# Performance work log

Hardware: AMD Instinct MI355X
Metric: run time of the kernel (lower is better)

## Reference

```python
import jax, jax.numpy as jnp
import numpy as np

L, S, B, E, H, FF = 512, 2048, 4, 1024, 16, 2048
HD = E // H  # 64


def _layernorm(x, g, b, eps=1e-5):
    m = jnp.mean(x, axis=-1, keepdims=True)
    v = jnp.mean((x - m) ** 2, axis=-1, keepdims=True)
    return (x - m) * jax.lax.rsqrt(v + eps) * g + b


def _decoder(tgt, memory, pos, query_pos,
             in_proj_w, in_proj_b, out_w, out_b,
             cq_w, cq_b, ck_w, ck_b, cv_w, cv_b,
             down_w, down_b, lin1_w, lin1_b, lin2_w, lin2_b,
             n1_g, n1_b, n2_g, n2_b, n3_g, n3_b):
    Lq, Bb, Em = tgt.shape
    scale = 1.0 / np.sqrt(HD).astype(np.float32)
    # --- self attention (torch nn.MultiheadAttention, eval mode, no masks) ---
    qk_in = tgt + query_pos
    Wq, Wk, Wv = jnp.split(in_proj_w, 3, axis=0)
    bq, bk, bv = jnp.split(in_proj_b, 3)
    q = (qk_in @ Wq.T + bq).reshape(Lq, Bb, H, HD)
    k = (qk_in @ Wk.T + bk).reshape(Lq, Bb, H, HD)
    v = (tgt @ Wv.T + bv).reshape(Lq, Bb, H, HD)
    attn = jax.nn.softmax(jnp.einsum('lbhd,mbhd->bhlm', q, k) * scale, axis=-1)
    ctx = jnp.einsum('bhlm,mbhd->lbhd', attn, v).reshape(Lq, Bb, Em)
    tgt = _layernorm(tgt + ctx @ out_w.T + out_b, n1_g, n1_b)
    # --- custom cross attention; inputs permuted to [B, E, N] (Conv1d k=1 == matmul) ---
    qc = jnp.einsum('oe,lbe->bol', cq_w, tgt + query_pos) + cq_b[None, :, None]
    kc = jnp.einsum('oe,sbe->bos', ck_w, memory + pos) + ck_b[None, :, None]
    vc = jnp.einsum('oe,sbe->bos', cv_w, memory) + cv_b[None, :, None]
    # view(B, head_dim, num_heads, N): channel axis splits as (HD, H)
    qc = qc.reshape(Bb, HD, H, -1)
    kc = kc.reshape(Bb, HD, H, -1)
    vc = vc.reshape(Bb, HD, H, -1)
    # scores_2[b,d,h,m] = kc[b,d,h,m] * sum_{d',n} qc[b,d',h,n] kc[b,d',h,m] / sqrt(HD)
    # (einsum('abcd,aced->abcd', key, scores_1) broadcasts key over the summed n axis)
    s1sum = jnp.einsum('bdh,bdhm->bhm', qc.sum(-1), kc) * scale
    prob = jax.nn.softmax(kc * s1sum[:, None, :, :], axis=-1)        # [B,HD,H,S]
    o = jnp.einsum('bnhm,bdhm->bdhn', prob, vc)                       # [B,HD,H,HD]
    o = (o @ down_w.T + down_b).reshape(Bb, Em, 1)                    # Linear HD->1, then view
    tgt = _layernorm(tgt + jnp.transpose(o, (2, 0, 1)), n2_g, n2_b)   # [1,B,E] broadcasts over L
    # --- FFN ---
    ff = jax.nn.relu(tgt @ lin1_w.T + lin1_b) @ lin2_w.T + lin2_b
    return _layernorm(tgt + ff, n3_g, n3_b)


def setup_inputs() -> dict:
    key = jax.random.key(0)
    ks = jax.random.split(key, 16)
    def nrm(k, shape, s=0.02):
        return (s * jax.random.normal(k, shape)).astype(jnp.float32)
    z = lambda *s: jnp.zeros(s, jnp.float32)
    return dict(
        tgt=nrm(ks[0], (L, B, E), 1.0),
        memory=nrm(ks[1], (S, B, E), 1.0),
        pos=nrm(ks[2], (S, B, E), 1.0),
        query_pos=nrm(ks[3], (L, B, E), 1.0),
        in_proj_w=nrm(ks[4], (3 * E, E)), in_proj_b=z(3 * E),
        out_w=nrm(ks[5], (E, E)), out_b=z(E),
        cq_w=nrm(ks[6], (E, E)), cq_b=z(E),
        ck_w=nrm(ks[7], (E, E)), ck_b=z(E),
        cv_w=nrm(ks[8], (E, E)), cv_b=z(E),
        down_w=nrm(ks[9], (1, HD)), down_b=z(1),
        lin1_w=nrm(ks[10], (FF, E)), lin1_b=z(FF),
        lin2_w=nrm(ks[11], (E, FF)), lin2_b=z(E),
        n1_g=jnp.ones((E,), jnp.float32), n1_b=z(E),
        n2_g=jnp.ones((E,), jnp.float32), n2_b=z(E),
        n3_g=jnp.ones((E,), jnp.float32), n3_b=z(E),
    )


def reference(tgt, memory, pos, query_pos,
              in_proj_w, in_proj_b, out_w, out_b,
              cq_w, cq_b, ck_w, ck_b, cv_w, cv_b,
              down_w, down_b, lin1_w, lin1_b, lin2_w, lin2_b,
              n1_g, n1_b, n2_g, n2_b, n3_g, n3_b):
    return _decoder(tgt, memory, pos, query_pos,
                    in_proj_w, in_proj_b, out_w, out_b,
                    cq_w, cq_b, ck_w, ck_b, cv_w, cv_b,
                    down_w, down_b, lin1_w, lin1_b, lin2_w, lin2_b,
                    n1_g, n1_b, n2_g, n2_b, n3_g, n3_b)
```

## Files before the change

### kernel.cpp

```cpp
#include <hip/hip_runtime.h>
#include <hip/hip_bf16.h>

typedef __hip_bfloat16 bf16;
typedef short short8 __attribute__((ext_vector_type(8)));
typedef float f32x4 __attribute__((ext_vector_type(4)));

#define Lq 512
#define Sm 2048
#define Bb 4
#define Ee 1024
#define Hh 16
#define FFd 2048
#define HDd 64

static __device__ __forceinline__ float b2f(bf16 x) { return __bfloat162float(x); }
static __device__ __forceinline__ bf16 f2b(float x) { return __float2bfloat16(x); }
static __device__ __forceinline__ unsigned short bits(bf16 x) {
    return __builtin_bit_cast(unsigned short, x);
}
static __device__ __forceinline__ float us2f(unsigned short u) {
    return b2f(__builtin_bit_cast(bf16, u));
}

static __device__ __forceinline__ void gload16(const void* g, void* l) {
    __builtin_amdgcn_global_load_lds(
        (const __attribute__((address_space(1))) unsigned int*)g,
        (__attribute__((address_space(3))) unsigned int*)l, 16, 0, 0);
}

__global__ __launch_bounds__(512, 2)
void kcvc_gemm(const bf16* __restrict__ wk, const bf16* __restrict__ wv,
               const bf16* __restrict__ mp, const bf16* __restrict__ mo,
               bf16* __restrict__ kc, bf16* __restrict__ vc,
               const float* __restrict__ kb, const float* __restrict__ vb)
{
    constexpr int BK = 64;
    __shared__ bf16 lA[2][256 * BK];
    __shared__ bf16 lB[2][256 * BK];

    const int tid  = threadIdx.x;
    const int lane = tid & 63;
    const int wm = (tid >> 6) >> 2;
    const int wn = (tid >> 6) & 3;

    int bid = (blockIdx.x & 7) * 32 + (blockIdx.x >> 3);
    const int bx = bid & 3;
    const int by = (bid >> 2) & 7;
    const int z  = bid >> 5;

    const bool isv = z >= 4;
    const int  b   = isv ? z - 4 : z;
    const bf16*  A    = isv ? wv : wk;
    const bf16*  B    = (isv ? mo : mp) + b * 1024;
    bf16*        C    = (isv ? vc : kc) + (long)b * 2097152;
    const float* bias = isv ? vb : kb;

    const int m0 = bx * 256, n0 = by * 256;
    const bf16* Abase = A + (long)m0 * 1024;
    const bf16* Bbase = B + (long)n0 * 4096;

    const int kgrp = lane >> 4, l16 = lane & 15;
    const int rsw = l16 & 7;

    auto stage = [&](int buf, int k0) {
#pragma unroll
        for (int r = 0; r < 4; r++) {
            int c = r * 512 + tid;
            int row = c >> 3;
            int ss = (c & 7) ^ (row & 7);
            gload16(Abase + (long)row * 1024 + k0 + ss * 8, &lA[buf][c * 8]);
        }
#pragma unroll
        for (int r = 0; r < 4; r++) {
            int c = r * 512 + tid;
            int row = c >> 3;
            int ss = (c & 7) ^ (row & 7);
            gload16(Bbase + (long)row * 4096 + k0 + ss * 8, &lB[buf][c * 8]);
        }
    };

    f32x4 acc[8][4];
#pragma unroll
    for (int i = 0; i < 8; i++)
#pragma unroll
        for (int j = 0; j < 4; j++) acc[i][j] = f32x4{0.f, 0.f, 0.f, 0.f};

    stage(0, 0);
    asm volatile("s_waitcnt vmcnt(0)" ::: "memory");
    __builtin_amdgcn_s_barrier();

    constexpr int NT = 16;
    for (int t = 0; t < NT; t++) {
        if (t + 1 < NT) stage((t + 1) & 1, (t + 1) * BK);

        const bf16* la = lA[t & 1];
        const bf16* lb = lB[t & 1];
#pragma unroll
        for (int h = 0; h < 2; h++) {
            const int sd = ((h * 4 + kgrp) ^ rsw) * 8;
            short8 af[8], bv[4];
#pragma unroll
            for (int i = 0; i < 8; i++)
                af[i] = *(const short8*)&la[(wm * 128 + i * 16 + l16) * BK + sd];
#pragma unroll
            for (int j = 0; j < 4; j++)
                bv[j] = *(const short8*)&lb[(wn * 64 + j * 16 + l16) * BK + sd];
            __builtin_amdgcn_s_setprio(1);
#pragma unroll
            for (int i = 0; i < 8; i++)
#pragma unroll
                for (int j = 0; j < 4; j++)
                    acc[i][j] = __builtin_amdgcn_mfma_f32_16x16x32_bf16(af[i], bv[j], acc[i][j], 0, 0, 0);
            __builtin_amdgcn_s_setprio(0);
        }

        asm volatile("s_waitcnt vmcnt(0)" ::: "memory");
        __builtin_amdgcn_s_barrier();
    }

#pragma unroll
    for (int i = 0; i < 8; i++) {
#pragma unroll
        for (int j = 0; j < 4; j++) {
#pragma unroll
            for (int r = 0; r < 4; r++) {
                int row = m0 + wm * 128 + i * 16 + kgrp * 4 + r;
                int col = n0 + wn * 64 + j * 16 + l16;
                float v = acc[i][j][r] + bias[row];
                float v2 = __shfl_xor(v, 1);
                if (!(l16 & 1)) {
                    unsigned int pk = (unsigned int)bits(f2b(v)) |
                                      ((unsigned int)bits(f2b(v2)) << 16);
                    *(unsigned int*)&C[(long)row * 2048 + col] = pk;
                }
            }
        }
    }
}

__global__ __launch_bounds__(512, 2)
void flash_attn(const bf16* __restrict__ qk, const bf16* __restrict__ vt,
                bf16* __restrict__ ctx)
{
    __shared__ bf16 lQ[128 * 64];
    __shared__ bf16 lK[2][64 * 64];
    __shared__ bf16 lV[2][64 * 64];
    __shared__ bf16 lP[128 * 64];
    __shared__ float scb[128];

    const int tid  = threadIdx.x;
    const int lane = tid & 63;
    const int wq   = tid >> 6;
    const int kgrp = lane >> 4, l16 = lane & 15;

    const int qt = blockIdx.x & 3;
    const int bh = blockIdx.x >> 2;
    const int b = bh >> 4, h = bh & 15;
    const int L0 = qt * 128;

#pragma unroll
    for (int it = 0; it < 2; it++) {
        int c = it * 512 + tid;
        int rr = c >> 3, sl = c & 7, ss = sl ^ (rr & 7);
        gload16(qk + ((long)(L0 + rr) * 4 + b) * 2048 + h * 64 + ss * 8,
                &lQ[(it * 512 + wq * 64) * 8]);
    }

    auto stageKV = [&](int buf, int st) {
        int rr = tid >> 3, sl = tid & 7, ss = sl ^ (rr & 7);
        gload16(qk + ((long)(st * 64 + rr) * 4 + b) * 2048 + 1024 + h * 64 + ss * 8,
                &lK[buf][(wq * 64) * 8]);
        gload16(vt + ((long)(b * 1024 + h * 64 + rr)) * 512 + st * 64 + ss * 8,
                &lV[buf][(wq * 64) * 8]);
    };

    auto frag = [&](const bf16* base, int row, int kk) {
        return *(const short8*)&base[row * 64 + (((kk * 4 + kgrp) ^ (l16 & 7)) * 8)];
    };

    f32x4 acc_o[4];
#pragma unroll
    for (int j = 0; j < 4; j++) acc_o[j] = f32x4{0.f, 0.f, 0.f, 0.f};
    float m_run = -1e30f, l_run = 0.f;

    stageKV(0, 0);
    asm volatile("s_waitcnt vmcnt(0)" ::: "memory");
    __builtin_amdgcn_s_barrier();

    int buf = 0;
    for (int st = 0; st < 8; st++) {
        if (st < 7) stageKV(buf ^ 1, st + 1);

        f32x4 accs[4];
#pragma unroll
        for (int fm = 0; fm < 4; fm++) accs[fm] = f32x4{0.f, 0.f, 0.f, 0.f};
        __builtin_amdgcn_s_setprio(1);
#pragma unroll
        for (int kk = 0; kk < 2; kk++) {
            short8 bq = frag(lQ, wq * 16 + l16, kk);
#pragma unroll
            for (int fm = 0; fm < 4; fm++) {
                short8 af = frag(lK[buf], fm * 16 + l16, kk);
                accs[fm] = __builtin_amdgcn_mfma_f32_16x16x32_bf16(af, bq, accs[fm], 0, 0, 0);
            }
        }
        __builtin_amdgcn_s_setprio(0);

        float v[4][4], p[4][4];
        float tmax = -1e30f;
#pragma unroll
        for (int fm = 0; fm < 4; fm++)
#pragma unroll
            for (int r = 0; r < 4; r++) {
                v[fm][r] = accs[fm][r] * 0.125f;
                tmax = fmaxf(tmax, v[fm][r]);
            }
        tmax = fmaxf(tmax, __shfl_xor(tmax, 16));
        tmax = fmaxf(tmax, __shfl_xor(tmax, 32));
        float m_new = fmaxf(m_run, tmax);
        float sc = __expf(m_run - m_new);
        float sum = 0.f;
#pragma unroll
        for (int fm = 0; fm < 4; fm++)
#pragma unroll
            for (int r = 0; r < 4; r++) {
                p[fm][r] = __expf(v[fm][r] - m_new);
                sum += p[fm][r];
            }
        sum += __shfl_xor(sum, 16);
        sum += __shfl_xor(sum, 32);
        l_run = l_run * sc + sum;
        m_run = m_new;

        if (!kgrp) scb[wq * 16 + l16] = sc;
        asm volatile("s_waitcnt lgkmcnt(0)" ::: "memory");
        __builtin_amdgcn_sched_barrier(0);
        float sc2[4];
#pragma unroll
        for (int r = 0; r < 4; r++) sc2[r] = scb[wq * 16 + kgrp * 4 + r];
#pragma unroll
        for (int fn = 0; fn < 4; fn++)
#pragma unroll
            for (int r = 0; r < 4; r++) acc_o[fn][r] *= sc2[r];

#pragma unroll
        for (int fm = 0; fm < 4; fm++) {
            int l = wq * 16 + l16;
            int sp = (fm * 2 + (kgrp >> 1)) ^ (l16 & 7);
            uint2 pk;
            pk.x = (unsigned int)bits(f2b(p[fm][0])) | ((unsigned int)bits(f2b(p[fm][1])) << 16);
            pk.y = (unsigned int)bits(f2b(p[fm][2])) | ((unsigned int)bits(f2b(p[fm][3])) << 16);
            *(uint2*)&lP[l * 64 + sp * 8 + (kgrp & 1) * 4] = pk;
        }
        asm volatile("s_waitcnt lgkmcnt(0)" ::: "memory");
        __builtin_amdgcn_sched_barrier(0);

        __builtin_amdgcn_s_setprio(1);
#pragma unroll
        for (int kk = 0; kk < 2; kk++) {
            short8 ap = frag(lP, wq * 16 + l16, kk);
#pragma unroll
            for (int fn = 0; fn < 4; fn++) {
                short8 bvf = frag(lV[buf], fn * 16 + l16, kk);
                acc_o[fn] = __builtin_amdgcn_mfma_f32_16x16x32_bf16(ap, bvf, acc_o[fn], 0, 0, 0);
            }
        }
        __builtin_amdgcn_s_setprio(0);

        asm volatile("s_waitcnt vmcnt(0)" ::: "memory");
        __builtin_amdgcn_s_barrier();
        buf ^= 1;
    }

    if (!kgrp) scb[wq * 16 + l16] = 1.f / l_run;
    asm volatile("s_waitcnt lgkmcnt(0)" ::: "memory");
    __builtin_amdgcn_sched_barrier(0);
    float inv[4];
#pragma unroll
    for (int r = 0; r < 4; r++) inv[r] = scb[wq * 16 + kgrp * 4 + r];
#pragma unroll
    for (int fn = 0; fn < 4; fn++) {
#pragma unroll
        for (int r = 0; r < 4; r++) {
            int lg = L0 + wq * 16 + kgrp * 4 + r;
            int d  = fn * 16 + l16;
            float vv = acc_o[fn][r] * inv[r];
            float v2 = __shfl_xor(vv, 1);
            if (!(l16 & 1)) {
                unsigned int pk = (unsigned int)bits(f2b(vv)) |
                                  ((unsigned int)bits(f2b(v2)) << 16);
                *(unsigned int*)&ctx[((long)lg * 4 + b) * 1024 + h * 64 + d] = pk;
            }
        }
    }
}

template<int BM, int BN>
__global__ __launch_bounds__(256)
void gemm_nt(const bf16* __restrict__ A, const bf16* __restrict__ Bw,
             float* __restrict__ Cf, bf16* __restrict__ Cb,
             const float* __restrict__ bias,
             const bf16* __restrict__ A2, const bf16* __restrict__ B2,
             bf16* __restrict__ Cb2, const float* __restrict__ bias2,
             int gx, int gy,
             int K, long lda, long ldb, long ldc,
             long sA1, long sA2, long sB1, long sB2, long sC1, long sC2,
             int zdiv, int zsplit, int nsplit, float alpha, int mode, int mode2)
{
    constexpr int BK = 32;
    constexpr int RA = BM / 64, RB = BN / 64;
    constexpr int NLOADS = RA + RB;
    __shared__ bf16 lA[3][BM * BK];
    __shared__ bf16 lB[3][BN * BK];

    const int tid  = threadIdx.x;
    const int lane = tid & 63;
    const int wave = tid >> 6;
    const int wm = wave >> 1, wn = wave & 1;
    constexpr int RM = BM / 2, RN = BN / 2;
    constexpr int FM = RM / 16, FN = RN / 16;

    const int nwg = gridDim.x;
    const int cpx = nwg >> 3;
    int bid = (blockIdx.x & 7) * cpx + (blockIdx.x >> 3);
    const int bx = bid % gx;
    int tmp = bid / gx;
    const int by = tmp % gy;
    const int z  = tmp / gy;

    const int m0 = bx * BM;
    const int n0 = by * BN;

    const bool use2 = (z >= zsplit) || (n0 >= nsplit);
    const int  zz   = (z >= zsplit) ? z - zsplit : z;
    const bf16*  Ap = (use2 && A2)    ? A2    : A;
    const bf16*  Bp = (use2 && B2)    ? B2    : Bw;
    const float* bp = (use2 && bias2) ? bias2 : bias;
    const int    md = use2 ? mode2 : mode;
    bf16*        Co = (use2 && Cb2)   ? Cb2   : Cb;

    const long offA = (long)(zz / zdiv) * sA1 + (long)(zz % zdiv) * sA2;
    const long offB = (long)(zz / zdiv) * sB1 + (long)(zz % zdiv) * sB2;
    const long offC = (long)(zz / zdiv) * sC1 + (long)(zz % zdiv) * sC2;

    const bf16* Abase = Ap + offA + (long)m0 * lda;
    const bf16* Bbase = Bp + offB + (long)n0 * ldb;

    const int kgrp = lane >> 4;
    const int l16  = lane & 15;

    const int swz   = (l16 >> 1) & 3;
    const int slotA = (kgrp ^ swz) * 8;

    auto stage = [&](int buf, int k0) {
#pragma unroll
        for (int r = 0; r < RA; r++) {
            int c = r * 256 + wave * 64 + lane;
            int row = c >> 2;
            int sslot = (c & 3) ^ ((row >> 1) & 3);
            gload16(Abase + (long)row * lda + k0 + sslot * 8,
                    &lA[buf][(r * 256 + wave * 64) * 8]);
        }
#pragma unroll
        for (int r = 0; r < RB; r++) {
            int c = r * 256 + wave * 64 + lane;
            int row = c >> 2;
            int sslot = (c & 3) ^ ((row >> 1) & 3);
            gload16(Bbase + (long)row * ldb + k0 + sslot * 8,
                    &lB[buf][(r * 256 + wave * 64) * 8]);
        }
    };

    f32x4 acc[FM][FN];
#pragma unroll
    for (int i = 0; i < FM; i++)
#pragma unroll
        for (int j = 0; j < FN; j++) acc[i][j] = f32x4{0.f, 0.f, 0.f, 0.f};

    const int nt = K / BK;
    stage(0, 0);
    if (nt > 1) {
        stage(1, BK);
        asm volatile("s_waitcnt vmcnt(%0)" :: "n"(NLOADS) : "memory");
    } else {
        asm volatile("s_waitcnt vmcnt(0)" ::: "memory");
    }
    __builtin_amdgcn_s_barrier();

    for (int t = 0; t < nt; t++) {
        const int cur = t % 3;
        if (t + 2 < nt) stage((t + 2) % 3, (t + 2) * BK);

        short8 af[FM], bv[FN];
#pragma unroll
        for (int i = 0; i < FM; i++)
            af[i] = *(const short8*)&lA[cur][(wm * RM + i * 16 + l16) * BK + slotA];
#pragma unroll
        for (int j = 0; j < FN; j++)
            bv[j] = *(const short8*)&lB[cur][(wn * RN + j * 16 + l16) * BK + slotA];
        __builtin_amdgcn_s_setprio(1);
#pragma unroll
        for (int i = 0; i < FM; i++)
#pragma unroll
            for (int j = 0; j < FN; j++)
                acc[i][j] = __builtin_amdgcn_mfma_f32_16x16x32_bf16(af[i], bv[j], acc[i][j], 0, 0, 0);
        __builtin_amdgcn_s_setprio(0);

        if (t + 2 < nt) {
            asm volatile("s_waitcnt vmcnt(%0)" :: "n"(NLOADS) : "memory");
        } else {
            asm volatile("s_waitcnt vmcnt(0)" ::: "memory");
        }
        __builtin_amdgcn_s_barrier();
    }

#pragma unroll
    for (int i = 0; i < FM; i++) {
#pragma unroll
        for (int j = 0; j < FN; j++) {
#pragma unroll
            for (int r = 0; r < 4; r++) {
                int row = m0 + wm * RM + i * 16 + kgrp * 4 + r;
                int col = n0 + wn * RN + j * 16 + l16;
                float v = alpha * acc[i][j][r] + (bp ? bp[col] : 0.f);
                float v2 = __shfl_xor(v, 1);
                if (md == 0) {
                    if (!(l16 & 1)) {
                        float2 pv = {v, v2};
                        *(float2*)&Cf[offC + (long)row * ldc + col] = pv;
                    }
                } else if (md == 1) {
                    if (!(l16 & 1)) {
                        unsigned int pk = (unsigned int)bits(f2b(v)) |
                                          ((unsigned int)bits(f2b(v2)) << 16);
                        *(unsigned int*)&Co[offC + (long)row * ldc + col] = pk;
                    }
                } else if (md == 2) {
                    if (!(l16 & 1)) {
                        unsigned int pk = (unsigned int)bits(f2b(fmaxf(v, 0.f))) |
                                          ((unsigned int)bits(f2b(fmaxf(v2, 0.f))) << 16);
                        *(unsigned int*)&Co[offC + (long)row * ldc + col] = pk;
                    }
                } else {
                    int o = col - nsplit;
                    Cb2[((long)(row & 3) * 1024 + o) * 512 + (row >> 2)] = f2b(v);
                }
            }
        }
    }
}

struct Cvt2Seg { const float* a; const float* b; bf16* d; bf16* d2; int nblk; };
struct Cvt2Args { Cvt2Seg s[8]; };

__global__ __launch_bounds__(256)
void cvt_kernel(Cvt2Args args)
{
    for (int ci = blockIdx.x; ci < 10240; ci += 2048) {
        int rem = ci;
        int si = 0;
        while (si < 7 && rem >= args.s[si].nblk) { rem -= args.s[si].nblk; si++; }
        Cvt2Seg sg = args.s[si];
        const long i = (long)rem * 2048 + threadIdx.x * 8;

        float4 a0 = *(const float4*)(sg.a + i);
        float4 a1 = *(const float4*)(sg.a + i + 4);
        float4 s0 = a0, s1 = a1;
        if (sg.b) {
            float4 b0 = *(const float4*)(sg.b + i);
            float4 b1 = *(const float4*)(sg.b + i + 4);
            s0.x += b0.x; s0.y += b0.y; s0.z += b0.z; s0.w += b0.w;
            s1.x += b1.x; s1.y += b1.y; s1.z += b1.z; s1.w += b1.w;
        }
        short8 u;
        u[0] = (short)bits(f2b(s0.x)); u[1] = (short)bits(f2b(s0.y));
        u[2] = (short)bits(f2b(s0.z)); u[3] = (short)bits(f2b(s0.w));
        u[4] = (short)bits(f2b(s1.x)); u[5] = (short)bits(f2b(s1.y));
        u[6] = (short)bits(f2b(s1.z)); u[7] = (short)bits(f2b(s1.w));
        *(short8*)((unsigned short*)sg.d + i) = u;
        if (sg.d2) {
            short8 w;
            w[0] = (short)bits(f2b(a0.x)); w[1] = (short)bits(f2b(a0.y));
            w[2] = (short)bits(f2b(a0.z)); w[3] = (short)bits(f2b(a0.w));
            w[4] = (short)bits(f2b(a1.x)); w[5] = (short)bits(f2b(a1.y));
            w[6] = (short)bits(f2b(a1.z)); w[7] = (short)bits(f2b(a1.w));
            *(short8*)((unsigned short*)sg.d2 + i) = w;
        }
    }
}

__global__ __launch_bounds__(256)
void ln_kernel(const float* __restrict__ x, const bf16* __restrict__ xB,
               const float* __restrict__ res, const float* __restrict__ resb,
               const float* __restrict__ g, const float* __restrict__ be,
               float* __restrict__ outF, bf16* __restrict__ outB)
{
    long row = blockIdx.x;
    int tid = threadIdx.x, lane = tid & 63, w = tid >> 6;
    float vv[4];
    if (x) {
        float4 xv = *(const float4*)(x + row * 1024 + tid * 4);
        vv[0] = xv.x; vv[1] = xv.y; vv[2] = xv.z; vv[3] = xv.w;
    } else {
        ushort4 xv = *(const ushort4*)((const unsigned short*)xB + row * 1024 + tid * 4);
        vv[0] = us2f(xv.x); vv[1] = us2f(xv.y); vv[2] = us2f(xv.z); vv[3] = us2f(xv.w);
    }
    if (res) {
        float4 rv = *(const float4*)(res + row * 1024 + tid * 4);
        vv[0] += rv.x; vv[1] += rv.y; vv[2] += rv.z; vv[3] += rv.w;
    }
    if (resb) {
        float4 rv = *(const float4*)(resb + (row & 3) * 1024 + tid * 4);
        vv[0] += rv.x; vv[1] += rv.y; vv[2] += rv.z; vv[3] += rv.w;
    }
    float s = vv[0] + vv[1] + vv[2] + vv[3];
    float q = vv[0] * vv[0] + vv[1] * vv[1] + vv[2] * vv[2] + vv[3] * vv[3];
    __shared__ float rs[4], rq[4];
    for (int o = 32; o; o >>= 1) { s += __shfl_xor(s, o); q += __shfl_xor(q, o); }
    if (!lane) { rs[w] = s; rq[w] = q; }
    __syncthreads();
    s = rs[0] + rs[1] + rs[2] + rs[3];
    q = rq[0] + rq[1] + rq[2] + rq[3];
    float mean = s * (1.f / 1024.f);
    float var  = q * (1.f / 1024.f) - mean * mean;
    float rstd = rsqrtf(var + 1e-5f);
    float4 gv = *(const float4*)(g + tid * 4);
    float4 bv = *(const float4*)(be + tid * 4);
    float o0 = (vv[0] - mean) * rstd * gv.x + bv.x;
    float o1 = (vv[1] - mean) * rstd * gv.y + bv.y;
    float o2 = (vv[2] - mean) * rstd * gv.z + bv.z;
    float o3 = (vv[3] - mean) * rstd * gv.w + bv.w;
    if (outF) {
        float4 ov = {o0, o1, o2, o3};
        *(float4*)(outF + row * 1024 + tid * 4) = ov;
    }
    if (outB) {
        ushort4 u;
        u.x = bits(f2b(o0)); u.y = bits(f2b(o1));
        u.z = bits(f2b(o2)); u.w = bits(f2b(o3));
        *reinterpret_cast<ushort4*>((unsigned short*)outB + row * 1024 + tid * 4) = u;
    }
}

__global__ __launch_bounds__(256)
void asum_part_kernel(const float* __restrict__ t1, const float* __restrict__ qp,
                      float* __restrict__ part)
{
    int blk = blockIdx.x;
    int lc = blk >> 4, b = (blk >> 2) & 3, ec = blk & 3;
    int e = ec * 256 + threadIdx.x;
    float acc = 0.f;
#pragma unroll 4
    for (int l = lc * 32; l < lc * 32 + 32; l++) {
        long idx = ((long)(l * 4 + b)) * 1024 + e;
        acc += t1[idx] + qp[idx];
    }
    part[(lc * 4 + b) * 1024 + e] = acc;
}

__global__ __launch_bounds__(256)
void asum_reduce_kernel(const float* __restrict__ part, float* __restrict__ asum)
{
    int b = blockIdx.x >> 2, ec = blockIdx.x & 3;
    int e = ec * 256 + threadIdx.x;
    float acc = 0.f;
#pragma unroll
    for (int lc = 0; lc < 16; lc++) acc += part[(lc * 4 + b) * 1024 + e];
    asum[b * 1024 + e] = acc;
}

__global__ __launch_bounds__(256)
void qsum_kernel(const float* __restrict__ cqw, const float* __restrict__ cqb,
                 const float* __restrict__ asum, float* __restrict__ qsum)
{
    int o = blockIdx.x * 4 + (threadIdx.x >> 6);
    int lane = threadIdx.x & 63;
    float a0 = 0, a1 = 0, a2 = 0, a3 = 0;
    for (int j = 0; j < 16; j++) {
        int e = lane + j * 64;
        float wv = cqw[(long)o * 1024 + e];
        a0 += wv * asum[e];
        a1 += wv * asum[1024 + e];
        a2 += wv * asum[2048 + e];
        a3 += wv * asum[3072 + e];
    }
    for (int t = 32; t; t >>= 1) {
        a0 += __shfl_xor(a0, t); a1 += __shfl_xor(a1, t);
        a2 += __shfl_xor(a2, t); a3 += __shfl_xor(a3, t);
    }
    if (!lane) {
        float bb = 512.f * cqb[o];
        qsum[o] = a0 + bb; qsum[1024 + o] = a1 + bb;
        qsum[2048 + o] = a2 + bb; qsum[3072 + o] = a3 + bb;
    }
}

__global__ __launch_bounds__(256)
void s1_kernel(const bf16* __restrict__ kc, const float* __restrict__ qsum,
               float* __restrict__ s1)
{
    int bh = blockIdx.x, b = bh >> 4, h = bh & 15;
    int m = blockIdx.y * 256 + threadIdx.x;
    __shared__ float qd[64];
    if (threadIdx.x < 64) qd[threadIdx.x] = qsum[b * 1024 + threadIdx.x * 16 + h];
    __syncthreads();
    const bf16* kcb = kc + (long)b * 2048 * 1024 + (long)h * 2048 + m;
    float acc = 0.f;
#pragma unroll 8
    for (int d = 0; d < 64; d++) acc += qd[d] * b2f(kcb[(long)d * 16 * 2048]);
    s1[(long)bh * 2048 + m] = acc * 0.125f;
}

__global__ __launch_bounds__(256)
void bsum_kernel(const bf16* __restrict__ kc, const float* __restrict__ s1,
                 float* __restrict__ rmax, float* __restrict__ rsum)
{
    int bh = blockIdx.x >> 6, n = blockIdx.x & 63;
    int b = bh >> 4, h = bh & 15;
    int tid = threadIdx.x, lane = tid & 63, w = tid >> 6;
    const bf16* row = kc + (long)b * 2048 * 1024 + (long)(n * 16 + h) * 2048;
    const float* s1r = s1 + (long)bh * 2048;
    float t[8];
    float mx = -1e30f;
#pragma unroll
    for (int i = 0; i < 8; i++) {
        int m = tid + i * 256;
        t[i] = b2f(row[m]) * s1r[m];
        mx = fmaxf(mx, t[i]);
    }
    __shared__ float redm[4], reds[4];
    for (int o = 32; o; o >>= 1) mx = fmaxf(mx, __shfl_xor(mx, o));
    if (!lane) redm[w] = mx;
    __syncthreads();
    mx = fmaxf(fmaxf(redm[0], redm[1]), fmaxf(redm[2], redm[3]));
    float s = 0.f;
#pragma unroll
    for (int i = 0; i < 8; i++) s += __expf(t[i] - mx);
    for (int o = 32; o; o >>= 1) s += __shfl_xor(s, o);
    if (!lane) reds[w] = s;
    __syncthreads();
    if (!tid) {
        rmax[bh * 64 + n] = mx;
        rsum[bh * 64 + n] = reds[0] + reds[1] + reds[2] + reds[3];
    }
}

__global__ __launch_bounds__(256)
void wpr_kernel(const bf16* __restrict__ kc, const float* __restrict__ s1,
                const float* __restrict__ rmax, const float* __restrict__ rsum,
                const float* __restrict__ dw, float* __restrict__ wpr)
{
    int bh = blockIdx.x, b = bh >> 4, h = bh & 15;
    int m = blockIdx.y * 256 + threadIdx.x;
    __shared__ float cf[64], cm[64];
    if (threadIdx.x < 64) {
        cf[threadIdx.x] = dw[threadIdx.x] / rsum[bh * 64 + threadIdx.x];
        cm[threadIdx.x] = rmax[bh * 64 + threadIdx.x];
    }
    __syncthreads();
    float s1v = s1[(long)bh * 2048 + m];
    const bf16* kcb = kc + (long)b * 2048 * 1024 + (long)h * 2048 + m;
    float acc = 0.f;
#pragma unroll 8
    for (int n = 0; n < 64; n++)
        acc += cf[n] * __expf(b2f(kcb[(long)n * 16 * 2048]) * s1v - cm[n]);
    wpr[(long)bh * 2048 + m] = acc;
}

__global__ __launch_bounds__(256)
void cout_kernel(const bf16* __restrict__ vc, const float* __restrict__ wpr,
                 const float* __restrict__ db, float* __restrict__ outs)
{
    int bh = blockIdx.x >> 2, dg = blockIdx.x & 3;
    int b = bh >> 4, h = bh & 15;
    int tid = threadIdx.x, lane = tid & 63, w = tid >> 6;
    __shared__ float lwpr[2048];
#pragma unroll
    for (int i = 0; i < 8; i++) lwpr[tid + i * 256] = wpr[(long)bh * 2048 + tid + i * 256];
    __syncthreads();
#pragma unroll
    for (int dd = 0; dd < 4; dd++) {
        int d = dg * 16 + w * 4 + dd;
        int o = d * 16 + h;
        const bf16* vrow = vc + (long)b * 2048 * 1024 + (long)o * 2048;
        float acc = 0.f;
#pragma unroll
        for (int j = 0; j < 4; j++) {
            int m = j * 512 + lane * 8;
            short8 vv = *(const short8*)&vrow[m];
#pragma unroll
            for (int k = 0; k < 8; k++) {
                bf16 bb = __builtin_bit_cast(bf16, (unsigned short)vv[k]);
                acc += lwpr[m + k] * b2f(bb);
            }
        }
        for (int t2 = 32; t2; t2 >>= 1) acc += __shfl_xor(acc, t2);
        if (!lane) outs[b * 1024 + o] = acc + db[0];
    }
}

extern "C" void kernel_launch(void* const* d_in, const int* in_sizes, int n_in,
                              void* d_out, int out_size, void* d_ws, size_t ws_size,
                              hipStream_t stream)
{
    const float* tgt  = (const float*)d_in[0];
    const float* mem  = (const float*)d_in[1];
    const float* pos  = (const float*)d_in[2];
    const float* qp   = (const float*)d_in[3];
    const float* ipw  = (const float*)d_in[4];
    const float* ipb  = (const float*)d_in[5];
    const float* outw = (const float*)d_in[6];
    const float* outb = (const float*)d_in[7];
    const float* cqw  = (const float*)d_in[8];
    const float* cqb  = (const float*)d_in[9];
    const float* ckw  = (const float*)d_in[10];
    const float* ckb  = (const float*)d_in[11];
    const float* cvw  = (const float*)d_in[12];
    const float* cvb  = (const float*)d_in[13];
    const float* dww  = (const float*)d_in[14];
    const float* dwb  = (const float*)d_in[15];
    const float* l1w  = (const float*)d_in[16];
    const float* l1b  = (const float*)d_in[17];
    const float* l2w  = (const float*)d_in[18];
    const float* l2b  = (const float*)d_in[19];
    const float* n1g  = (const float*)d_in[20];
    const float* n1b  = (const float*)d_in[21];
    const float* n2g  = (const float*)d_in[22];
    const float* n2b  = (const float*)d_in[23];
    const float* n3g  = (const float*)d_in[24];
    const float* n3b  = (const float*)d_in[25];

    char* ws = (char*)d_ws;
    auto MB = [](long x) { return x << 20; };
    bf16* w_ip    = (bf16*)(ws + MB(0));
    bf16* w_out   = (bf16*)(ws + MB(6));
    bf16* w_ck    = (bf16*)(ws + MB(8));
    bf16* w_cv    = (bf16*)(ws + MB(10));
    bf16* w_l1    = (bf16*)(ws + MB(12));
    bf16* w_l2    = (bf16*)(ws + MB(16));
    bf16* qkin    = (bf16*)(ws + MB(20));
    bf16* tgtb    = (bf16*)(ws + MB(24));
    bf16* memposb = (bf16*)(ws + MB(28));
    bf16* memb    = (bf16*)(ws + MB(44));
    bf16* qkbuf   = (bf16*)(ws + MB(60));
    bf16* vtb     = (bf16*)(ws + MB(68));
    bf16* kcb     = (bf16*)(ws + MB(72));
    bf16* ctxb    = (bf16*)(ws + MB(104));
    bf16* atmpb   = (bf16*)(ws + MB(108));
    float* s1buf  = (float*)(ws + MB(108));
    float* wprbuf = (float*)(ws + MB(109));
    float* rmax   = (float*)(ws + MB(110));
    float* rsum   = (float*)(ws + MB(110) + (64 << 10));
    float* part   = (float*)(ws + MB(111));
    float* tgt1   = (float*)(ws + MB(116));
    float* asum   = (float*)(ws + MB(124));
    float* qsum   = (float*)(ws + MB(125));
    bf16* vcb     = (bf16*)(ws + MB(126));
    float* outs   = (float*)(ws + MB(142));
    float* tgt2   = (float*)(ws + MB(143));
    bf16* tgt2b   = (bf16*)(ws + MB(151));
    bf16* ff1b    = (bf16*)(ws + MB(155));
    bf16* ff2b    = (bf16*)(ws + MB(163));

    const int BIGZ = 1000000, BIGN = 1 << 30;

    Cvt2Args ca{};
    ca.s[0] = {ipw,  nullptr, w_ip,    nullptr, 1536};
    ca.s[1] = {outw, nullptr, w_out,   nullptr, 512};
    ca.s[2] = {ckw,  nullptr, w_ck,    nullptr, 512};
    ca.s[3] = {cvw,  nullptr, w_cv,    nullptr, 512};
    ca.s[4] = {l1w,  nullptr, w_l1,    nullptr, 1024};
    ca.s[5] = {l2w,  nullptr, w_l2,    nullptr, 1024};
    ca.s[6] = {tgt,  qp,      qkin,    tgtb,    1024};
    ca.s[7] = {mem,  pos,     memposb, memb,    4096};
    cvt_kernel<<<dim3(2048, 1, 1), 256, 0, stream>>>(ca);

    gemm_nt<64, 128><<<dim3(768, 1, 1), 256, 0, stream>>>(
        qkin, w_ip, nullptr, qkbuf, ipb,
        tgtb, nullptr, vtb, nullptr,
        32, 24,
        1024, 1024, 1024, 2048,
        0, 0, 0, 0, 0, 0, 1, BIGZ, 2048, 1.f, 1, 3);

    flash_attn<<<dim3(256, 1, 1), 512, 0, stream>>>(qkbuf, vtb, ctxb);

    gemm_nt<64, 128><<<dim3(256, 1, 1), 256, 0, stream>>>(
        ctxb, w_out, nullptr, atmpb, outb,
        nullptr, nullptr, nullptr, nullptr,
        32, 8,
        1024, 1024, 1024, 1024,
        0, 0, 0, 0, 0, 0, 1, BIGZ, BIGN, 1.f, 1, 1);

    ln_kernel<<<dim3(2048, 1, 1), 256, 0, stream>>>(
        nullptr, atmpb, tgt, nullptr, n1g, n1b, tgt1, nullptr);

    asum_part_kernel<<<dim3(256, 1, 1), 256, 0, stream>>>(tgt1, qp, part);
    asum_reduce_kernel<<<dim3(16, 1, 1), 256, 0, stream>>>(part, asum);
    qsum_kernel<<<dim3(256, 1, 1), 256, 0, stream>>>(cqw, cqb, asum, qsum);

    kcvc_gemm<<<dim3(256, 1, 1), 512, 0, stream>>>(
        w_ck, w_cv, memposb, memb, kcb, vcb, ckb, cvb);

    s1_kernel<<<dim3(64, 8, 1), 256, 0, stream>>>(kcb, qsum, s1buf);
    bsum_kernel<<<dim3(4096, 1, 1), 256, 0, stream>>>(kcb, s1buf, rmax, rsum);
    wpr_kernel<<<dim3(64, 8, 1), 256, 0, stream>>>(kcb, s1buf, rmax, rsum, dww, wprbuf);
    cout_kernel<<<dim3(256, 1, 1), 256, 0, stream>>>(vcb, wprbuf, dwb, outs);

    ln_kernel<<<dim3(2048, 1, 1), 256, 0, stream>>>(
        tgt1, nullptr, nullptr, outs, n2g, n2b, tgt2, tgt2b);

    gemm_nt<64, 128><<<dim3(512, 1, 1), 256, 0, stream>>>(
        tgt2b, w_l1, nullptr, ff1b, l1b,
        nullptr, nullptr, nullptr, nullptr,
        32, 16,
        1024, 1024, 1024, 2048,
        0, 0, 0, 0, 0, 0, 1, BIGZ, BIGN, 1.f, 2, 2);

    gemm_nt<64, 128><<<dim3(256, 1, 1), 256, 0, stream>>>(
        ff1b, w_l2, nullptr, ff2b, l2b,
        nullptr, nullptr, nullptr, nullptr,
        32, 8,
        2048, 2048, 2048, 1024,
        0, 0, 0, 0, 0, 0, 1, BIGZ, BIGN, 1.f, 1, 1);

    ln_kernel<<<dim3(2048, 1, 1), 256, 0, stream>>>(
        nullptr, ff2b, tgt2, nullptr, n3g, n3b, (float*)d_out, nullptr);
}
```

Before: 272.6 us.

## Switch GEMM to BK=64 double-buffered LDS pipeline with 8-slot XOR swizzle

Changes the GEMM main loop from a triple-buffered K=32 pipeline to a double-buffered K=64 pipeline. Each stage loads twice as much and the loop issues two MFMA sub-steps per barrier, which halves the number of barriers and waitcnts per K. The LDS swizzle is widened to 8 slots to fit the 64-element rows. The cost is a shallower prefetch (one stage ahead instead of two) and possibly a larger LDS footprint, which can expose global-load latency and lower occupancy.

```diff
diff --git a/kernel.cpp b/kernel.cpp
--- a/kernel.cpp
+++ b/kernel.cpp
@@ -307,11 +307,10 @@
              long sA1, long sA2, long sB1, long sB2, long sC1, long sC2,
              int zdiv, int zsplit, int nsplit, float alpha, int mode, int mode2)
 {
-    constexpr int BK = 32;
-    constexpr int RA = BM / 64, RB = BN / 64;
-    constexpr int NLOADS = RA + RB;
-    __shared__ bf16 lA[3][BM * BK];
-    __shared__ bf16 lB[3][BN * BK];
+    constexpr int BK = 64;
+    constexpr int RA = BM / 32, RB = BN / 32;
+    __shared__ bf16 lA[2][BM * BK];
+    __shared__ bf16 lB[2][BN * BK];
 
     const int tid  = threadIdx.x;
     const int lane = tid & 63;
@@ -348,26 +347,22 @@
 
     const int kgrp = lane >> 4;
     const int l16  = lane & 15;
-
-    const int swz   = (l16 >> 1) & 3;
-    const int slotA = (kgrp ^ swz) * 8;
+    const int rsw  = l16 & 7;
 
     auto stage = [&](int buf, int k0) {
 #pragma unroll
         for (int r = 0; r < RA; r++) {
-            int c = r * 256 + wave * 64 + lane;
-            int row = c >> 2;
-            int sslot = (c & 3) ^ ((row >> 1) & 3);
-            gload16(Abase + (long)row * lda + k0 + sslot * 8,
-                    &lA[buf][(r * 256 + wave * 64) * 8]);
+            int c = r * 256 + tid;
+            int row = c >> 3;
+            int ss = (c & 7) ^ (row & 7);
+            gload16(Abase + (long)row * lda + k0 + ss * 8, &lA[buf][c * 8]);
         }
 #pragma unroll
         for (int r = 0; r < RB; r++) {
-            int c = r * 256 + wave * 64 + lane;
-            int row = c >> 2;
-            int sslot = (c & 3) ^ ((row >> 1) & 3);
-            gload16(Bbase + (long)row * ldb + k0 + sslot * 8,
-                    &lB[buf][(r * 256 + wave * 64) * 8]);
+            int c = r * 256 + tid;
+            int row = c >> 3;
+            int ss = (c & 7) ^ (row & 7);
+            gload16(Bbase + (long)row * ldb + k0 + ss * 8, &lB[buf][c * 8]);
         }
     };
 
@@ -379,38 +374,34 @@
 
     const int nt = K / BK;
     stage(0, 0);
-    if (nt > 1) {
-        stage(1, BK);
-        asm volatile("s_waitcnt vmcnt(%0)" :: "n"(NLOADS) : "memory");
-    } else {
+    asm volatile("s_waitcnt vmcnt(0)" ::: "memory");
+    __builtin_amdgcn_s_barrier();
+
+    for (int t = 0; t < nt; t++) {
+        if (t + 1 < nt) stage((t + 1) & 1, (t + 1) * BK);
+
+        const bf16* la = lA[t & 1];
+        const bf16* lb = lB[t & 1];
+#pragma unroll
+        for (int h = 0; h < 2; h++) {
+            const int sd = ((h * 4 + kgrp) ^ rsw) * 8;
+            short8 af[FM], bv[FN];
+#pragma unroll
+            for (int i = 0; i < FM; i++)
+                af[i] = *(const short8*)&la[(wm * RM + i * 16 + l16) * BK + sd];
+#pragma unroll
+            for (int j = 0; j < FN; j++)
+                bv[j] = *(const short8*)&lb[(wn * RN + j * 16 + l16) * BK + sd];
+            __builtin_amdgcn_s_setprio(1);
+#pragma unroll
+            for (int i = 0; i < FM; i++)
+#pragma unroll
+                for (int j = 0; j < FN; j++)
+                    acc[i][j] = __builtin_amdgcn_mfma_f32_16x16x32_bf16(af[i], bv[j], acc[i][j], 0, 0, 0);
+            __builtin_amdgcn_s_setprio(0);
+        }
+
         asm volatile("s_waitcnt vmcnt(0)" ::: "memory");
-    }
-    __builtin_amdgcn_s_barrier();
-
-    for (int t = 0; t < nt; t++) {
-        const int cur = t % 3;
-        if (t + 2 < nt) stage((t + 2) % 3, (t + 2) * BK);
-
-        short8 af[FM], bv[FN];
-#pragma unroll
-        for (int i = 0; i < FM; i++)
-            af[i] = *(const short8*)&lA[cur][(wm * RM + i * 16 + l16) * BK + slotA];
-#pragma unroll
-        for (int j = 0; j < FN; j++)
-            bv[j] = *(const short8*)&lB[cur][(wn * RN + j * 16 + l16) * BK + slotA];
-        __builtin_amdgcn_s_setprio(1);
-#pragma unroll
-        for (int i = 0; i < FM; i++)
-#pragma unroll
-            for (int j = 0; j < FN; j++)
-                acc[i][j] = __builtin_amdgcn_mfma_f32_16x16x32_bf16(af[i], bv[j], acc[i][j], 0, 0, 0);
-        __builtin_amdgcn_s_setprio(0);
-
-        if (t + 2 < nt) {
-            asm volatile("s_waitcnt vmcnt(%0)" :: "n"(NLOADS) : "memory");
-        } else {
-            asm volatile("s_waitcnt vmcnt(0)" ::: "memory");
-        }
         __builtin_amdgcn_s_barrier();
     }
 
```

New measurement: 257.8 us. 5.4% less time.
